# Optimization experiments

Measured on AMD Instinct MI355X. Metric: run time of the kernel, lower is better.

Reference implementation:

```python
import jax, jax.numpy as jnp
import numpy as np

DATA_SZ = 1000   # number of timesteps, from source: data_sz = 1000
BATCH = 1024
DIM = 64
HIDDEN = 256


def setup_inputs() -> dict:
    key = jax.random.key(0)
    k0, k1, k2, k3, k4 = jax.random.split(key, 5)
    y0 = jax.random.normal(k0, (BATCH, DIM), dtype=jnp.float32)
    t = jnp.linspace(0.0, 15.0, DATA_SZ).astype(jnp.float32)
    W1 = jax.random.normal(k1, (DIM, HIDDEN), dtype=jnp.float32) * (1.0 / np.sqrt(DIM))
    b1 = jax.random.normal(k2, (HIDDEN,), dtype=jnp.float32) * 0.01
    W2 = jax.random.normal(k3, (HIDDEN, DIM), dtype=jnp.float32) * (1.0 / np.sqrt(HIDDEN))
    b2 = jax.random.normal(k4, (DIM,), dtype=jnp.float32) * 0.01
    return {"y0": y0, "t": t, "W1": W1, "b1": b1, "W2": W2, "b2": b2}


def reference(y0, t, W1, b1, W2, b2):
    # func: autonomous tanh-MLP vector field f(t, y) = tanh(y@W1+b1)@W2+b2
    def func(ti, y):
        return jnp.tanh(y @ W1 + b1) @ W2 + b2

    # solver: classic RK4 step returning dy (matches solver(func, t0, h, y0) -> dy)
    def rk4_dy(t0, h, y):
        half = h * 0.5
        k1 = func(t0, y)
        k2 = func(t0 + half, y + half * k1)
        k3 = func(t0 + half, y + half * k2)
        k4 = func(t0 + h, y + h * k3)
        return (h / 6.0) * (k1 + 2.0 * k2 + 2.0 * k3 + k4)

    ts = t[:-1]
    hs = t[1:] - t[:-1]

    def step(y, th):
        t0, h = th
        y1 = y + rk4_dy(t0, h, y)
        return y1, y1

    _, ys = jax.lax.scan(step, y0, (ts, hs))  # ys: [T-1, B, D]
    return jnp.concatenate([y0[None], ys], axis=0)  # [T, B, D]
```

## Files before the change

kernel.cpp:

```cpp
#include <hip/hip_runtime.h>


#define NB 1024
#define ND 64
#define NH 256
#define NBLK 512
#define NTHR 512

#define XBOF(C,W) (((C)<<8) + ((W)<<6))
#define ABOF(C)   (512 + ((C)<<8))
#define PTOF(C)   (1024 + (C)*320)

#define R64(M) M(0) M(1) M(2) M(3) M(4) M(5) M(6) M(7) M(8) M(9) \
  M(10) M(11) M(12) M(13) M(14) M(15) M(16) M(17) M(18) M(19) \
  M(20) M(21) M(22) M(23) M(24) M(25) M(26) M(27) M(28) M(29) \
  M(30) M(31) M(32) M(33) M(34) M(35) M(36) M(37) M(38) M(39) \
  M(40) M(41) M(42) M(43) M(44) M(45) M(46) M(47) M(48) M(49) \
  M(50) M(51) M(52) M(53) M(54) M(55) M(56) M(57) M(58) M(59) \
  M(60) M(61) M(62) M(63)

#define Q16(M) M(0,0,1,2,3) M(1,4,5,6,7) M(2,8,9,10,11) M(3,12,13,14,15) \
  M(4,16,17,18,19) M(5,20,21,22,23) M(6,24,25,26,27) M(7,28,29,30,31) \
  M(8,32,33,34,35) M(9,36,37,38,39) M(10,40,41,42,43) M(11,44,45,46,47) \
  M(12,48,49,50,51) M(13,52,53,54,55) M(14,56,57,58,59) M(15,60,61,62,63)

__device__ __forceinline__ float fast_tanh(float x) {
    float e = __expf(2.0f * x);
    float r = __builtin_amdgcn_rcpf(e + 1.0f);
    return 1.0f - 2.0f * r;
}

#define BSYNC() do {                                             \
    asm volatile("s_waitcnt lgkmcnt(0)" ::: "memory");           \
    __builtin_amdgcn_s_barrier();                                \
    asm volatile("" ::: "memory");                               \
} while (0)

__global__ __launch_bounds__(NTHR, 4)
void node_rk4_kernel(const float* __restrict__ y0,
                     const float* __restrict__ t,
                     const float* W1,
                     const float* b1,
                     const float* W2,
                     const float* b2,
                     float* __restrict__ out,
                     int nsteps)
{
    __shared__ float lds[1664];
    const int tid = threadIdx.x;
    const int w   = tid >> 6;
    const int l   = tid & 63;

    if (w < 4) {
        const int j = (w << 6) + l;
        const float b1l = b1[j];
        const float b2l = b2[l];
        #define DW1(i) float w1_##i;
        R64(DW1)
        #define LW1(i) w1_##i = W1[(i) * NH + j];
        R64(LW1)

        float* xbwA = lds + XBOF(0, w);
        float* xbwB = lds + XBOF(1, w);
        const float4* xqA = (const float4*)xbwA;
        const float4* xqB = (const float4*)xbwB;
        float* abA = lds + ABOF(0) + (w << 6);
        float* abB = lds + ABOF(1) + (w << 6);
        const float* prA = lds + PTOF(0);
        const float* prB = lds + PTOF(1);

        const int row0 = blockIdx.x * 2;
        float yA = y0[(row0 + 0) * ND + l];
        float yB = y0[(row0 + 1) * ND + l];
        float kaA = 0.0f, kaB = 0.0f;
        if (w == 0) {
            out[(size_t)(row0 + 0) * ND + l] = yA;
            out[(size_t)(row0 + 1) * ND + l] = yB;
        }
        float dt = 0.0f, dt2 = 0.0f, dt6 = 0.0f;
        size_t obase = 0;

#define G1Q(q,i0,i1,i2,i3) { float4 xv_ = xq_[q]; \
    h0_ = fmaf(w1_##i0, xv_.x, h0_); h1_ = fmaf(w1_##i1, xv_.y, h1_); \
    h0_ = fmaf(w1_##i2, xv_.z, h0_); h1_ = fmaf(w1_##i3, xv_.w, h1_); }

#define G1SLOT(C, CI, ST) do {                                       \
    float x_;                                                        \
    if ((ST) == 0) { x_ = y##C; }                                    \
    else {                                                           \
      const float* pr_ = pr##C + l * 5;                              \
      float kc_ = ((pr_[0] + pr_[1]) + (pr_[2] + pr_[3])) + b2l;     \
      if ((ST)==1)      { ka##C  = kc_;       x_ = fmaf(dt2, kc_, y##C); } \
      else if ((ST)==2) { ka##C += 2.0f*kc_;  x_ = fmaf(dt2, kc_, y##C); } \
      else if ((ST)==3) { ka##C += 2.0f*kc_;  x_ = fmaf(dt,  kc_, y##C); } \
      else { y##C = fmaf(dt6, ka##C + kc_, y##C); x_ = y##C;         \
             if (w == 0) out[obase + (CI) * ND + l] = y##C; }        \
    }                                                                \
    xbw##C[l] = x_;                                                  \
    asm volatile("s_waitcnt lgkmcnt(0)" ::: "memory");               \
    const float4* xq_ = xq##C;                                       \
    float h0_ = b1l, h1_ = 0.0f;                                     \
    Q16(G1Q)                                                         \
    ab##C[l] = fast_tanh(h0_ + h1_);                                 \
} while (0)

        G1SLOT(A, 0, 0); BSYNC();
        G1SLOT(B, 1, 0); BSYNC();
        for (int s = 0; s < nsteps; ++s) {
            dt = t[s + 1] - t[s]; dt2 = 0.5f * dt; dt6 = dt * (1.0f / 6.0f);
            obase = (size_t)(s + 1) * (NB * ND) + (size_t)row0 * ND;
            G1SLOT(A, 0, 1); BSYNC();  G1SLOT(B, 1, 1); BSYNC();
            G1SLOT(A, 0, 2); BSYNC();  G1SLOT(B, 1, 2); BSYNC();
            G1SLOT(A, 0, 3); BSYNC();  G1SLOT(B, 1, 3); BSYNC();
            G1SLOT(A, 0, 4); BSYNC();  G1SLOT(B, 1, 4); BSYNC();
        }
    } else {
        const int jj = w - 4;
        #define DW2(i) float w2_##i;
        R64(DW2)
        #define LW2(i) w2_##i = W2[((jj << 6) + (i)) * ND + l];
        R64(LW2)

        const float4* aqA = (const float4*)(lds + ABOF(0) + (jj << 6));
        const float4* aqB = (const float4*)(lds + ABOF(1) + (jj << 6));
        float* pwA = lds + PTOF(0);
        float* pwB = lds + PTOF(1);

#define G2Q(q,i0,i1,i2,i3) { float4 av_ = aq_[q]; \
    p0_ = fmaf(w2_##i0, av_.x, p0_); p1_ = fmaf(w2_##i1, av_.y, p1_); \
    p0_ = fmaf(w2_##i2, av_.z, p0_); p1_ = fmaf(w2_##i3, av_.w, p1_); }

#define G2SLOT(C) do {                                               \
    const float4* aq_ = aq##C;                                       \
    float p0_ = 0.0f, p1_ = 0.0f;                                    \
    Q16(G2Q)                                                         \
    pw##C[l * 5 + jj] = p0_ + p1_;      \
} while (0)

        BSYNC();
        G2SLOT(A); BSYNC();
        for (int s = 0; s < nsteps; ++s) {
            G2SLOT(B); BSYNC();  G2SLOT(A); BSYNC();
            G2SLOT(B); BSYNC();  G2SLOT(A); BSYNC();
            G2SLOT(B); BSYNC();  G2SLOT(A); BSYNC();
            G2SLOT(B); BSYNC();  G2SLOT(A); BSYNC();
        }
    }
}

extern "C" void kernel_launch(void* const* d_in, const int* in_sizes, int n_in,
                              void* d_out, int out_size, void* d_ws, size_t ws_size,
                              hipStream_t stream) {
    const float* y0 = (const float*)d_in[0];
    const float* t  = (const float*)d_in[1];
    const float* W1 = (const float*)d_in[2];
    const float* b1 = (const float*)d_in[3];
    const float* W2 = (const float*)d_in[4];
    const float* b2 = (const float*)d_in[5];
    float* out = (float*)d_out;
    int nsteps = in_sizes[1] - 1;
    hipLaunchKernelGGL(node_rk4_kernel, dim3(NBLK), dim3(NTHR), 0, stream,
                       y0, t, W1, b1, W2, b2, out, nsteps);
}
```

Before: 4.674 ms.

## Process four batch rows per block so each weight register feeds two FMAs

Each block now handles four batch rows instead of two: each pipeline slot carries two rows, and each register-resident W1/W2 weight is applied to both. The grid is halved to 256 blocks, LDS buffers are doubled, and launch bounds go from 4 to 2 blocks per SM. The aim is to halve the number of barrier-separated serial slots per unit of work and to spread LDS-read and barrier overhead over more FMAs. The cost is fewer blocks, which lowers latency hiding and may leave some CUs idle with only 256 blocks.

```diff
diff --git a/kernel.cpp b/kernel.cpp
--- a/kernel.cpp
+++ b/kernel.cpp
@@ -4,12 +4,13 @@
 #define NB 1024
 #define ND 64
 #define NH 256
-#define NBLK 512
+#define NBLK 256
 #define NTHR 512
 
-#define XBOF(C,W) (((C)<<8) + ((W)<<6))
-#define ABOF(C)   (512 + ((C)<<8))
-#define PTOF(C)   (1024 + (C)*320)
+#define XBOF(C,W) (((C)<<9) + ((W)<<7))
+#define ABOF(C)   (1024 + ((C)<<9))
+#define PTOF(C)   (2048 + (C)*640)
+#define LDS_FL 3328
 
 #define R64(M) M(0) M(1) M(2) M(3) M(4) M(5) M(6) M(7) M(8) M(9) \
   M(10) M(11) M(12) M(13) M(14) M(15) M(16) M(17) M(18) M(19) \
@@ -36,7 +37,7 @@
     asm volatile("" ::: "memory");                               \
 } while (0)
 
-__global__ __launch_bounds__(NTHR, 4)
+__global__ __launch_bounds__(NTHR, 2)
 void node_rk4_kernel(const float* __restrict__ y0,
                      const float* __restrict__ t,
                      const float* W1,
@@ -46,7 +47,7 @@
                      float* __restrict__ out,
                      int nsteps)
 {
-    __shared__ float lds[1664];
+    __shared__ float lds[LDS_FL];
     const int tid = threadIdx.x;
     const int w   = tid >> 6;
     const int l   = tid & 63;
@@ -60,59 +61,71 @@
         #define LW1(i) w1_##i = W1[(i) * NH + j];
         R64(LW1)
 
-        float* xbwA = lds + XBOF(0, w);
-        float* xbwB = lds + XBOF(1, w);
-        const float4* xqA = (const float4*)xbwA;
-        const float4* xqB = (const float4*)xbwB;
-        float* abA = lds + ABOF(0) + (w << 6);
-        float* abB = lds + ABOF(1) + (w << 6);
-        const float* prA = lds + PTOF(0);
-        const float* prB = lds + PTOF(1);
+        float* xbA = lds + XBOF(0, w);
+        float* xbB = lds + XBOF(1, w);
+        float* abA = lds + ABOF(0);
+        float* abB = lds + ABOF(1);
+        const float* ptA = lds + PTOF(0);
+        const float* ptB = lds + PTOF(1);
 
-        const int row0 = blockIdx.x * 2;
-        float yA = y0[(row0 + 0) * ND + l];
-        float yB = y0[(row0 + 1) * ND + l];
-        float kaA = 0.0f, kaB = 0.0f;
+        const int row0 = blockIdx.x * 4;
+        float yA0 = y0[(row0 + 0) * ND + l], yA1 = y0[(row0 + 1) * ND + l];
+        float yB0 = y0[(row0 + 2) * ND + l], yB1 = y0[(row0 + 3) * ND + l];
+        float kaA0 = 0.f, kaA1 = 0.f, kaB0 = 0.f, kaB1 = 0.f;
         if (w == 0) {
-            out[(size_t)(row0 + 0) * ND + l] = yA;
-            out[(size_t)(row0 + 1) * ND + l] = yB;
+            out[(size_t)(row0 + 0) * ND + l] = yA0;
+            out[(size_t)(row0 + 1) * ND + l] = yA1;
+            out[(size_t)(row0 + 2) * ND + l] = yB0;
+            out[(size_t)(row0 + 3) * ND + l] = yB1;
         }
-        float dt = 0.0f, dt2 = 0.0f, dt6 = 0.0f;
+        float dt = 0.f, dt2 = 0.f, dt6 = 0.f;
         size_t obase = 0;
 
-#define G1Q(q,i0,i1,i2,i3) { float4 xv_ = xq_[q]; \
-    h0_ = fmaf(w1_##i0, xv_.x, h0_); h1_ = fmaf(w1_##i1, xv_.y, h1_); \
-    h0_ = fmaf(w1_##i2, xv_.z, h0_); h1_ = fmaf(w1_##i3, xv_.w, h1_); }
+#define G1Q(q,i0,i1,i2,i3) { float4 xa_ = xq0_[q], xb_ = xq1_[q]; \
+    h0a = fmaf(w1_##i0, xa_.x, h0a); h0b = fmaf(w1_##i0, xb_.x, h0b); \
+    h1a = fmaf(w1_##i1, xa_.y, h1a); h1b = fmaf(w1_##i1, xb_.y, h1b); \
+    h0a = fmaf(w1_##i2, xa_.z, h0a); h0b = fmaf(w1_##i2, xb_.z, h0b); \
+    h1a = fmaf(w1_##i3, xa_.w, h1a); h1b = fmaf(w1_##i3, xb_.w, h1b); }
 
-#define G1SLOT(C, CI, ST) do {                                       \
-    float x_;                                                        \
-    if ((ST) == 0) { x_ = y##C; }                                    \
-    else {                                                           \
-      const float* pr_ = pr##C + l * 5;                              \
-      float kc_ = ((pr_[0] + pr_[1]) + (pr_[2] + pr_[3])) + b2l;     \
-      if ((ST)==1)      { ka##C  = kc_;       x_ = fmaf(dt2, kc_, y##C); } \
-      else if ((ST)==2) { ka##C += 2.0f*kc_;  x_ = fmaf(dt2, kc_, y##C); } \
-      else if ((ST)==3) { ka##C += 2.0f*kc_;  x_ = fmaf(dt,  kc_, y##C); } \
-      else { y##C = fmaf(dt6, ka##C + kc_, y##C); x_ = y##C;         \
-             if (w == 0) out[obase + (CI) * ND + l] = y##C; }        \
-    }                                                                \
-    xbw##C[l] = x_;                                                  \
-    asm volatile("s_waitcnt lgkmcnt(0)" ::: "memory");               \
-    const float4* xq_ = xq##C;                                       \
-    float h0_ = b1l, h1_ = 0.0f;                                     \
-    Q16(G1Q)                                                         \
-    ab##C[l] = fast_tanh(h0_ + h1_);                                 \
+#define G1SLOT(C, CB, ST) do {                                        \
+    float x0_, x1_;                                                   \
+    if ((ST) == 0) { x0_ = y##C##0; x1_ = y##C##1; }                  \
+    else {                                                            \
+      const float* pr0_ = pt##C + l * 5;                              \
+      const float* pr1_ = pt##C + 320 + l * 5;                        \
+      float k0_ = ((pr0_[0]+pr0_[1]) + (pr0_[2]+pr0_[3])) + b2l;      \
+      float k1_ = ((pr1_[0]+pr1_[1]) + (pr1_[2]+pr1_[3])) + b2l;      \
+      if ((ST)==1)      { ka##C##0 = k0_;        ka##C##1 = k1_;      \
+          x0_ = fmaf(dt2,k0_,y##C##0); x1_ = fmaf(dt2,k1_,y##C##1); } \
+      else if ((ST)==2) { ka##C##0 += 2.0f*k0_;  ka##C##1 += 2.0f*k1_;\
+          x0_ = fmaf(dt2,k0_,y##C##0); x1_ = fmaf(dt2,k1_,y##C##1); } \
+      else if ((ST)==3) { ka##C##0 += 2.0f*k0_;  ka##C##1 += 2.0f*k1_;\
+          x0_ = fmaf(dt,k0_,y##C##0);  x1_ = fmaf(dt,k1_,y##C##1); }  \
+      else { y##C##0 = fmaf(dt6, ka##C##0 + k0_, y##C##0);            \
+             y##C##1 = fmaf(dt6, ka##C##1 + k1_, y##C##1);            \
+             x0_ = y##C##0; x1_ = y##C##1;                            \
+             if (w == 0) { out[obase + (CB)*ND + l]       = y##C##0;  \
+                           out[obase + ((CB)+1)*ND + l]   = y##C##1; } } \
+    }                                                                 \
+    xb##C[l] = x0_; xb##C[64 + l] = x1_;                              \
+    asm volatile("s_waitcnt lgkmcnt(0)" ::: "memory");                \
+    const float4* xq0_ = (const float4*)xb##C;                        \
+    const float4* xq1_ = (const float4*)(xb##C + 64);                 \
+    float h0a = b1l, h1a = 0.0f, h0b = b1l, h1b = 0.0f;               \
+    Q16(G1Q)                                                          \
+    ab##C[j]       = fast_tanh(h0a + h1a);                            \
+    ab##C[256 + j] = fast_tanh(h0b + h1b);                            \
 } while (0)
 
         G1SLOT(A, 0, 0); BSYNC();
-        G1SLOT(B, 1, 0); BSYNC();
+        G1SLOT(B, 2, 0); BSYNC();
         for (int s = 0; s < nsteps; ++s) {
             dt = t[s + 1] - t[s]; dt2 = 0.5f * dt; dt6 = dt * (1.0f / 6.0f);
             obase = (size_t)(s + 1) * (NB * ND) + (size_t)row0 * ND;
-            G1SLOT(A, 0, 1); BSYNC();  G1SLOT(B, 1, 1); BSYNC();
-            G1SLOT(A, 0, 2); BSYNC();  G1SLOT(B, 1, 2); BSYNC();
-            G1SLOT(A, 0, 3); BSYNC();  G1SLOT(B, 1, 3); BSYNC();
-            G1SLOT(A, 0, 4); BSYNC();  G1SLOT(B, 1, 4); BSYNC();
+            G1SLOT(A, 0, 1); BSYNC();  G1SLOT(B, 2, 1); BSYNC();
+            G1SLOT(A, 0, 2); BSYNC();  G1SLOT(B, 2, 2); BSYNC();
+            G1SLOT(A, 0, 3); BSYNC();  G1SLOT(B, 2, 3); BSYNC();
+            G1SLOT(A, 0, 4); BSYNC();  G1SLOT(B, 2, 4); BSYNC();
         }
     } else {
         const int jj = w - 4;
@@ -121,20 +134,25 @@
         #define LW2(i) w2_##i = W2[((jj << 6) + (i)) * ND + l];
         R64(LW2)
 
-        const float4* aqA = (const float4*)(lds + ABOF(0) + (jj << 6));
-        const float4* aqB = (const float4*)(lds + ABOF(1) + (jj << 6));
+        const float4* aqA0 = (const float4*)(lds + ABOF(0) + (jj << 6));
+        const float4* aqA1 = (const float4*)(lds + ABOF(0) + 256 + (jj << 6));
+        const float4* aqB0 = (const float4*)(lds + ABOF(1) + (jj << 6));
+        const float4* aqB1 = (const float4*)(lds + ABOF(1) + 256 + (jj << 6));
         float* pwA = lds + PTOF(0);
         float* pwB = lds + PTOF(1);
 
-#define G2Q(q,i0,i1,i2,i3) { float4 av_ = aq_[q]; \
-    p0_ = fmaf(w2_##i0, av_.x, p0_); p1_ = fmaf(w2_##i1, av_.y, p1_); \
-    p0_ = fmaf(w2_##i2, av_.z, p0_); p1_ = fmaf(w2_##i3, av_.w, p1_); }
+#define G2Q(q,i0,i1,i2,i3) { float4 aa_ = aq0_[q], ab_ = aq1_[q]; \
+    p0a = fmaf(w2_##i0, aa_.x, p0a); p0b = fmaf(w2_##i0, ab_.x, p0b); \
+    p1a = fmaf(w2_##i1, aa_.y, p1a); p1b = fmaf(w2_##i1, ab_.y, p1b); \
+    p0a = fmaf(w2_##i2, aa_.z, p0a); p0b = fmaf(w2_##i2, ab_.z, p0b); \
+    p1a = fmaf(w2_##i3, aa_.w, p1a); p1b = fmaf(w2_##i3, ab_.w, p1b); }
 
 #define G2SLOT(C) do {                                               \
-    const float4* aq_ = aq##C;                                       \
-    float p0_ = 0.0f, p1_ = 0.0f;                                    \
+    const float4* aq0_ = aq##C##0; const float4* aq1_ = aq##C##1;    \
+    float p0a = 0.f, p1a = 0.f, p0b = 0.f, p1b = 0.f;                \
     Q16(G2Q)                                                         \
-    pw##C[l * 5 + jj] = p0_ + p1_;      \
+    pw##C[l * 5 + jj]       = p0a + p1a;         \
+    pw##C[320 + l * 5 + jj] = p0b + p1b;                             \
 } while (0)
 
         BSYNC();
```

New measurement: 5.530 ms. 1.18x slower.

## Split both MLP GEMVs across twice as many waves with half-K reductions

Applied to the files above, without the earlier changes.

Doubles the block to 1024 threads so 8 waves compute the first layer, each lane handling half of the input dimension, with the halves combined via a cross-lane shuffle. 8 waves compute the second layer over 32 hidden units each, and the partial sums are reduced over 8 slots instead of 4. This halves the serial FMA chain and per-thread register weights in each RK4 stage, shortening the latency-bound per-step critical path. In exchange it adds shuffle and reduction work, larger barriers across 16 waves, and relaxes the occupancy hint in the launch bounds.

```diff
diff --git a/kernel.cpp b/kernel.cpp
--- a/kernel.cpp
+++ b/kernel.cpp
@@ -5,24 +5,19 @@
 #define ND 64
 #define NH 256
 #define NBLK 512
-#define NTHR 512
+#define NTHR 1024
 
-#define XBOF(C,W) (((C)<<8) + ((W)<<6))
-#define ABOF(C)   (512 + ((C)<<8))
-#define PTOF(C)   (1024 + (C)*320)
+#define XBOF(C,W) (((C)<<9) + ((W)<<6))
+#define ABOF(C)   (1024 + ((C)<<8))
+#define PTOF(C)   (1536 + (C)*576)
+#define LDS_FL 2688
 
-#define R64(M) M(0) M(1) M(2) M(3) M(4) M(5) M(6) M(7) M(8) M(9) \
+#define R32(M) M(0) M(1) M(2) M(3) M(4) M(5) M(6) M(7) M(8) M(9) \
   M(10) M(11) M(12) M(13) M(14) M(15) M(16) M(17) M(18) M(19) \
-  M(20) M(21) M(22) M(23) M(24) M(25) M(26) M(27) M(28) M(29) \
-  M(30) M(31) M(32) M(33) M(34) M(35) M(36) M(37) M(38) M(39) \
-  M(40) M(41) M(42) M(43) M(44) M(45) M(46) M(47) M(48) M(49) \
-  M(50) M(51) M(52) M(53) M(54) M(55) M(56) M(57) M(58) M(59) \
-  M(60) M(61) M(62) M(63)
+  M(20) M(21) M(22) M(23) M(24) M(25) M(26) M(27) M(28) M(29) M(30) M(31)
 
-#define Q16(M) M(0,0,1,2,3) M(1,4,5,6,7) M(2,8,9,10,11) M(3,12,13,14,15) \
-  M(4,16,17,18,19) M(5,20,21,22,23) M(6,24,25,26,27) M(7,28,29,30,31) \
-  M(8,32,33,34,35) M(9,36,37,38,39) M(10,40,41,42,43) M(11,44,45,46,47) \
-  M(12,48,49,50,51) M(13,52,53,54,55) M(14,56,57,58,59) M(15,60,61,62,63)
+#define Q8(M) M(0,0,1,2,3) M(1,4,5,6,7) M(2,8,9,10,11) M(3,12,13,14,15) \
+  M(4,16,17,18,19) M(5,20,21,22,23) M(6,24,25,26,27) M(7,28,29,30,31)
 
 __device__ __forceinline__ float fast_tanh(float x) {
     float e = __expf(2.0f * x);
@@ -36,7 +31,7 @@
     asm volatile("" ::: "memory");                               \
 } while (0)
 
-__global__ __launch_bounds__(NTHR, 4)
+__global__ __launch_bounds__(NTHR)
 void node_rk4_kernel(const float* __restrict__ y0,
                      const float* __restrict__ t,
                      const float* W1,
@@ -46,26 +41,25 @@
                      float* __restrict__ out,
                      int nsteps)
 {
-    __shared__ float lds[1664];
+    __shared__ float lds[LDS_FL];
     const int tid = threadIdx.x;
     const int w   = tid >> 6;
     const int l   = tid & 63;
 
-    if (w < 4) {
-        const int j = (w << 6) + l;
-        const float b1l = b1[j];
+    if (w < 8) {
+        const int u    = (w << 5) + (l & 31);
+        const int kh32 = (l >> 5) << 5;
+        const float b1u = b1[u];
         const float b2l = b2[l];
         #define DW1(i) float w1_##i;
-        R64(DW1)
-        #define LW1(i) w1_##i = W1[(i) * NH + j];
-        R64(LW1)
+        R32(DW1)
+        #define LW1(i) w1_##i = W1[(kh32 + (i)) * NH + u];
+        R32(LW1)
 
         float* xbwA = lds + XBOF(0, w);
         float* xbwB = lds + XBOF(1, w);
-        const float4* xqA = (const float4*)xbwA;
-        const float4* xqB = (const float4*)xbwB;
-        float* abA = lds + ABOF(0) + (w << 6);
-        float* abB = lds + ABOF(1) + (w << 6);
+        float* abA  = lds + ABOF(0);
+        float* abB  = lds + ABOF(1);
         const float* prA = lds + PTOF(0);
         const float* prB = lds + PTOF(1);
 
@@ -88,8 +82,9 @@
     float x_;                                                        \
     if ((ST) == 0) { x_ = y##C; }                                    \
     else {                                                           \
-      const float* pr_ = pr##C + l * 5;                              \
-      float kc_ = ((pr_[0] + pr_[1]) + (pr_[2] + pr_[3])) + b2l;     \
+      const float* pr_ = pr##C + l * 9;                              \
+      float kc_ = (((pr_[0] + pr_[1]) + (pr_[2] + pr_[3]))           \
+                +  ((pr_[4] + pr_[5]) + (pr_[6] + pr_[7]))) + b2l;   \
       if ((ST)==1)      { ka##C  = kc_;       x_ = fmaf(dt2, kc_, y##C); } \
       else if ((ST)==2) { ka##C += 2.0f*kc_;  x_ = fmaf(dt2, kc_, y##C); } \
       else if ((ST)==3) { ka##C += 2.0f*kc_;  x_ = fmaf(dt,  kc_, y##C); } \
@@ -98,10 +93,12 @@
     }                                                                \
     xbw##C[l] = x_;                                                  \
     asm volatile("s_waitcnt lgkmcnt(0)" ::: "memory");               \
-    const float4* xq_ = xq##C;                                       \
-    float h0_ = b1l, h1_ = 0.0f;                                     \
-    Q16(G1Q)                                                         \
-    ab##C[l] = fast_tanh(h0_ + h1_);                                 \
+    const float4* xq_ = (const float4*)(xbw##C + kh32);              \
+    float h0_ = 0.0f, h1_ = 0.0f;                                    \
+    Q8(G1Q)                                                          \
+    float hp_ = h0_ + h1_;                                           \
+    float ho_ = __shfl_xor(hp_, 32, 64);                             \
+    ab##C[u] = fast_tanh((hp_ + ho_) + b1u);                         \
 } while (0)
 
         G1SLOT(A, 0, 0); BSYNC();
@@ -115,14 +112,14 @@
             G1SLOT(A, 0, 4); BSYNC();  G1SLOT(B, 1, 4); BSYNC();
         }
     } else {
-        const int jj = w - 4;
+        const int g2 = w - 8;
         #define DW2(i) float w2_##i;
-        R64(DW2)
-        #define LW2(i) w2_##i = W2[((jj << 6) + (i)) * ND + l];
-        R64(LW2)
+        R32(DW2)
+        #define LW2(i) w2_##i = W2[((g2 << 5) + (i)) * ND + l];
+        R32(LW2)
 
-        const float4* aqA = (const float4*)(lds + ABOF(0) + (jj << 6));
-        const float4* aqB = (const float4*)(lds + ABOF(1) + (jj << 6));
+        const float4* aqA = (const float4*)(lds + ABOF(0) + (g2 << 5));
+        const float4* aqB = (const float4*)(lds + ABOF(1) + (g2 << 5));
         float* pwA = lds + PTOF(0);
         float* pwB = lds + PTOF(1);
 
@@ -133,8 +130,8 @@
 #define G2SLOT(C) do {                                               \
     const float4* aq_ = aq##C;                                       \
     float p0_ = 0.0f, p1_ = 0.0f;                                    \
-    Q16(G2Q)                                                         \
-    pw##C[l * 5 + jj] = p0_ + p1_;      \
+    Q8(G2Q)                                                          \
+    pw##C[l * 9 + g2] = p0_ + p1_;    \
 } while (0)
 
         BSYNC();
```

Measured after the change: 7.050 ms. 1.51x slower.
